# Performance work log

Hardware: AMD Instinct MI355X
Metric: run time of the kernel (lower is better)

Reference implementation:

```python
import jax, jax.numpy as jnp
import numpy as np

N = 100000          # nodes
E = 1600000         # edges (avg degree 16)
D_IN = 128          # in_features
D_OUT = 128         # out_features


def setup_inputs() -> dict:
    key = jax.random.key(0)
    k1, k2, k3, k4 = jax.random.split(key, 4)
    H = jax.random.normal(k1, (N, D_IN), dtype=jnp.float32)
    # COO indices of sparse adjacency A: row i aggregates features of col j
    src = jax.random.randint(k2, (E,), 0, N, dtype=jnp.int32)
    dst = jax.random.randint(k3, (E,), 0, N, dtype=jnp.int32)
    # nn.Linear(2*in_features, out_features): weight [out, 2*in], zero bias
    W = jax.random.normal(k4, (D_OUT, 2 * D_IN), dtype=jnp.float32) * 0.05
    b = jnp.zeros((D_OUT,), dtype=jnp.float32)
    return {"H": H, "src": src, "dst": dst, "W": W, "b": b}


def reference(H, src, dst, W, b):
    # max-aggregation: for each node i, max over features of its neighbors.
    # One fused gather + segment-max replaces the per-node Python loop.
    gathered = H[dst]  # [E, D_IN]
    agg = jax.ops.segment_max(gathered, src, num_segments=N)  # [N, D_IN]
    # nodes with no incoming edges stay zero (torch code leaves zeros)
    deg = jax.ops.segment_sum(jnp.ones((src.shape[0],), jnp.float32), src,
                              num_segments=N)  # [N]
    H_neigh = jnp.where(deg[:, None] > 0, agg, 0.0)
    H_concat = jnp.concatenate([H, H_neigh], axis=1)  # [N, 2*D_IN]
    return H_concat @ W.T + b
```

## Files before the change

kernel.cpp:

```cpp
#include <hip/hip_runtime.h>
#include <math.h>

#define NN 100000
#define NE 1600000
#define DD 128
#define NB 1563
#define CAP 1280
#define PB 196
#define CB 196

#define WS_HH  0
#define WS_CUR 6400000
#define WS_ENT (WS_CUR + NB)
#define WS_AH  (WS_ENT + NB * CAP)
#define WS_WH  (WS_AH + NN * (DD / 2))

typedef __attribute__((ext_vector_type(8))) _Float16 h8_t;
typedef __attribute__((ext_vector_type(4))) _Float16 h4_t;
typedef __attribute__((ext_vector_type(2))) _Float16 h2_t;
typedef __attribute__((ext_vector_type(4))) float f4_t;

__device__ __forceinline__ unsigned pk2h(float x, float y) {
    h2_t h;
    h.x = (_Float16)x;
    h.y = (_Float16)y;
    return *(unsigned*)&h;
}

__device__ __forceinline__ h4_t h4max(h4_t a, h4_t b) {
    return __builtin_elementwise_max(a, b);
}

__global__ __launch_bounds__(1024) void init_kernel(const float* __restrict__ W,
                                                    unsigned* __restrict__ Wh,
                                                    int* __restrict__ cursor) {
    int i = blockIdx.x * 1024 + threadIdx.x;
    if (i < 128 * 256 / 2) Wh[i] = pk2h(W[2 * i], W[2 * i + 1]);
    int j = i - 128 * 256 / 2;
    if (j >= 0 && j < NB) cursor[j] = 0;
}

__global__ __launch_bounds__(1024) void prep_kernel(const float* __restrict__ H,
                                                    const int* __restrict__ src,
                                                    const int* __restrict__ dst,
                                                    int* __restrict__ cursor,
                                                    unsigned* __restrict__ entries,
                                                    uint4* __restrict__ Hh4) {
    __shared__ int cnt[NB];
    __shared__ int gcur[NB];
    const int t = threadIdx.x;
    const int b = blockIdx.x;
    if (b < PB) {
        for (int i = t; i < NB; i += 1024) cnt[i] = 0;
        __syncthreads();
        const int base = b * 8192;
        int sv[8];
#pragma unroll
        for (int k = 0; k < 8; ++k) {
            int e = base + k * 1024 + t;
            sv[k] = (e < NE) ? src[e] : -1;
            if (sv[k] >= 0) atomicAdd(&cnt[sv[k] >> 6], 1);
        }
        __syncthreads();
        for (int i = t; i < NB; i += 1024) {
            int c = cnt[i];
            gcur[i] = c ? i * CAP + atomicAdd(&cursor[i], c) : 0;
        }
        __syncthreads();
#pragma unroll
        for (int k = 0; k < 8; ++k) {
            int e = base + k * 1024 + t;
            if (sv[k] >= 0) {
                int s = sv[k];
                int pos = atomicAdd(&gcur[s >> 6], 1);
                entries[pos] = ((unsigned)(s & 63) << 17) | (unsigned)dst[e];
            }
        }
    } else {
        const int nb = b - PB;
        const int n8 = NN * DD / 8;
        for (int i = nb * 1024 + t; i < n8; i += CB * 1024) {
            const float4* s = (const float4*)H + (size_t)i * 2;
            float4 a = s[0], c4 = s[1];
            uint4 o;
            o.x = pk2h(a.x, a.y);
            o.y = pk2h(a.z, a.w);
            o.z = pk2h(c4.x, c4.y);
            o.w = pk2h(c4.z, c4.w);
            Hh4[i] = o;
        }
    }
}

__global__ __launch_bounds__(256) void agg_kernel(const _Float16* __restrict__ Hh,
                                                  const int* __restrict__ cursor,
                                                  const unsigned* __restrict__ entries,
                                                  unsigned* __restrict__ Ah) {
    __shared__ unsigned raw[CAP];
    __shared__ unsigned sorted[CAP];
    __shared__ int cnt[64], base_s[64], cur[64];
    const int t = threadIdx.x;
    const int b = blockIdx.x;
    const int n = cursor[b];

    if (t < 64) cnt[t] = 0;
    __syncthreads();
    for (int i = t; i < n; i += 256) {
        unsigned e = entries[b * CAP + i];
        raw[i] = e;
        atomicAdd(&cnt[e >> 17], 1);
    }
    __syncthreads();
    if (t < 64) {
        int v = cnt[t];
        int incl = v;
#pragma unroll
        for (int o = 1; o < 64; o <<= 1) {
            int y = __shfl_up(incl, o, 64);
            if (t >= o) incl += y;
        }
        base_s[t] = incl - v;
        cur[t] = incl - v;
    }
    __syncthreads();
    for (int i = t; i < n; i += 256) {
        unsigned e = raw[i];
        int pos = atomicAdd(&cur[e >> 17], 1);
        sorted[pos] = e & 0x1FFFFu;
    }
    __syncthreads();

    const int lane = t & 63;
    const int w = t >> 6;
    const int half = lane >> 5;
    const int l32 = lane & 31;
    const _Float16* __restrict__ colbase = Hh + l32 * 4;
#pragma unroll
    for (int q = 0; q < 16; ++q) {
        int ln = w * 16 + q;
        int s0 = base_s[ln];
        int e0 = s0 + cnt[ln];
        unsigned long long mu = 0xFC00FC00FC00FC00ull;
        h4_t m = *(h4_t*)&mu;
        int j = s0 + half;
        for (; j + 6 < e0; j += 8) {
            int d0 = sorted[j], d1 = sorted[j + 2];
            int d2 = sorted[j + 4], d3 = sorted[j + 6];
            h4_t v0 = *(const h4_t*)(colbase + (size_t)d0 * DD);
            h4_t v1 = *(const h4_t*)(colbase + (size_t)d1 * DD);
            h4_t v2 = *(const h4_t*)(colbase + (size_t)d2 * DD);
            h4_t v3 = *(const h4_t*)(colbase + (size_t)d3 * DD);
            m = h4max(m, h4max(h4max(v0, v1), h4max(v2, v3)));
        }
        for (; j < e0; j += 2) {
            h4_t v0 = *(const h4_t*)(colbase + (size_t)sorted[j] * DD);
            m = h4max(m, v0);
        }
        uint2 mv = *(uint2*)&m;
        uint2 ov;
        ov.x = (unsigned)__shfl_xor((int)mv.x, 32, 64);
        ov.y = (unsigned)__shfl_xor((int)mv.y, 32, 64);
        h4_t om = *(h4_t*)&ov;
        m = h4max(m, om);
        int node = b * 64 + ln;
        if (half == 0 && node < NN) {
            uint2 outv = make_uint2(0u, 0u);
            if (s0 < e0) outv = *(uint2*)&m;
            *(uint2*)(Ah + (size_t)node * 64 + l32 * 2) = outv;
        }
    }
}

#define XP 72
__global__ __launch_bounds__(256) void mfma_matmul_kernel(
        const unsigned short* __restrict__ Hh,
        const unsigned short* __restrict__ Ah,
        const unsigned short* __restrict__ Wh,
        const float* __restrict__ bias,
        float* __restrict__ out) {
    __shared__ unsigned short Xs[128 * XP];
    __shared__ unsigned short Ws[128 * XP];
    const int t = threadIdx.x;
    const int lane = t & 63;
    const int w = t >> 6;
    const int quad = lane >> 4;
    const int l16 = lane & 15;
    const int blockrow = blockIdx.x * 128;

    f4_t acc[2][8] = {};

    for (int c = 0; c < 4; ++c) {
        const int k0 = c * 64;
        {
            const unsigned short* xb = (c < 2) ? Hh : Ah;
            const int koff = (c < 2) ? k0 : k0 - 128;
            const int seg = t & 7, r0 = t >> 3;
#pragma unroll
            for (int j = 0; j < 4; ++j) {
                int r = r0 + 32 * j;
                int row = blockrow + r;
                uint4 v = make_uint4(0, 0, 0, 0);
                if (row < NN)
                    v = *(const uint4*)(xb + (size_t)row * DD + koff + seg * 8);
                *(uint4*)&Xs[r * XP + seg * 8] = v;
            }
        }
        {
            const int seg = t & 7, o0 = t >> 3;
#pragma unroll
            for (int j = 0; j < 4; ++j) {
                int o = o0 + 32 * j;
                uint4 v = *(const uint4*)(Wh + (size_t)o * 256 + k0 + seg * 8);
                *(uint4*)&Ws[o * XP + seg * 8] = v;
            }
        }
        __syncthreads();
#pragma unroll
        for (int kk = 0; kk < 64; kk += 32) {
            h8_t a0 = *(const h8_t*)&Xs[(w * 32 + l16) * XP + kk + quad * 8];
            h8_t a1 = *(const h8_t*)&Xs[(w * 32 + 16 + l16) * XP + kk + quad * 8];
#pragma unroll
            for (int ot = 0; ot < 8; ++ot) {
                h8_t bf = *(const h8_t*)&Ws[(ot * 16 + l16) * XP + kk + quad * 8];
                acc[0][ot] = __builtin_amdgcn_mfma_f32_16x16x32_f16(a0, bf, acc[0][ot], 0, 0, 0);
                acc[1][ot] = __builtin_amdgcn_mfma_f32_16x16x32_f16(a1, bf, acc[1][ot], 0, 0, 0);
            }
        }
        __syncthreads();
    }

#pragma unroll
    for (int ot = 0; ot < 8; ++ot) {
        float bv = bias[ot * 16 + l16];
#pragma unroll
        for (int sub = 0; sub < 2; ++sub) {
#pragma unroll
            for (int reg = 0; reg < 4; ++reg) {
                int row = blockrow + w * 32 + sub * 16 + quad * 4 + reg;
                if (row < NN)
                    out[(size_t)row * DD + ot * 16 + l16] = acc[sub][ot][reg] + bv;
            }
        }
    }
}

extern "C" void kernel_launch(void* const* d_in, const int* in_sizes, int n_in,
                              void* d_out, int out_size, void* d_ws, size_t ws_size,
                              hipStream_t stream) {
    const float* H   = (const float*)d_in[0];
    const int*   src = (const int*)d_in[1];
    const int*   dst = (const int*)d_in[2];
    const float* W   = (const float*)d_in[3];
    const float* b   = (const float*)d_in[4];
    float* out = (float*)d_out;

    int* ws = (int*)d_ws;
    unsigned short* Hh      = (unsigned short*)(ws + WS_HH);
    int*            cursor  = ws + WS_CUR;
    unsigned*       entries = (unsigned*)(ws + WS_ENT);
    unsigned*       Ah      = (unsigned*)(ws + WS_AH);
    unsigned*       Wh      = (unsigned*)(ws + WS_WH);

    init_kernel<<<18, 1024, 0, stream>>>(W, Wh, cursor);
    prep_kernel<<<PB + CB, 1024, 0, stream>>>(H, src, dst, cursor, entries, (uint4*)Hh);
    agg_kernel<<<NB, 256, 0, stream>>>((const _Float16*)Hh, cursor, entries, Ah);
    mfma_matmul_kernel<<<(NN + 127) / 128, 256, 0, stream>>>(
        Hh, (const unsigned short*)Ah, (const unsigned short*)Wh, b, out);
}
```

Before: 238.3 us.

## Fuse neighbor max-aggregation with MFMA matmul and fold weight conversion into prep

Merges the aggregation kernel and the matmul kernel so each 64-node block keeps its aggregated half-precision features and its own H rows in shared memory, then runs the MFMA GEMM directly on them. This removes the global write and re-read of the aggregated buffer and one kernel launch. The weight-conversion init kernel is folded into an extra prep block and the cursor reset becomes a memset. The trade-off is a smaller 64-row matmul tile per block, so weights are reloaded once per 64 rows instead of per 128, and shared memory use rises, which may lower occupancy during the gather phase.

```diff
diff --git a/kernel.cpp b/kernel.cpp
--- a/kernel.cpp
+++ b/kernel.cpp
@@ -12,8 +12,7 @@
 #define WS_HH  0
 #define WS_CUR 6400000
 #define WS_ENT (WS_CUR + NB)
-#define WS_AH  (WS_ENT + NB * CAP)
-#define WS_WH  (WS_AH + NN * (DD / 2))
+#define WS_WH  (WS_ENT + NB * CAP)
 
 typedef __attribute__((ext_vector_type(8))) _Float16 h8_t;
 typedef __attribute__((ext_vector_type(4))) _Float16 h4_t;
@@ -31,21 +30,14 @@
     return __builtin_elementwise_max(a, b);
 }
 
-__global__ __launch_bounds__(1024) void init_kernel(const float* __restrict__ W,
-                                                    unsigned* __restrict__ Wh,
-                                                    int* __restrict__ cursor) {
-    int i = blockIdx.x * 1024 + threadIdx.x;
-    if (i < 128 * 256 / 2) Wh[i] = pk2h(W[2 * i], W[2 * i + 1]);
-    int j = i - 128 * 256 / 2;
-    if (j >= 0 && j < NB) cursor[j] = 0;
-}
-
 __global__ __launch_bounds__(1024) void prep_kernel(const float* __restrict__ H,
                                                     const int* __restrict__ src,
                                                     const int* __restrict__ dst,
                                                     int* __restrict__ cursor,
                                                     unsigned* __restrict__ entries,
-                                                    uint4* __restrict__ Hh4) {
+                                                    uint4* __restrict__ Hh4,
+                                                    const float* __restrict__ W,
+                                                    unsigned* __restrict__ Wh) {
     __shared__ int cnt[NB];
     __shared__ int gcur[NB];
     const int t = threadIdx.x;
@@ -76,7 +68,7 @@
                 entries[pos] = ((unsigned)(s & 63) << 17) | (unsigned)dst[e];
             }
         }
-    } else {
+    } else if (b < PB + CB) {
         const int nb = b - PB;
         const int n8 = NN * DD / 8;
         for (int i = nb * 1024 + t; i < n8; i += CB * 1024) {
@@ -89,15 +81,26 @@
             o.w = pk2h(c4.z, c4.w);
             Hh4[i] = o;
         }
-    }
-}
-
-__global__ __launch_bounds__(256) void agg_kernel(const _Float16* __restrict__ Hh,
-                                                  const int* __restrict__ cursor,
-                                                  const unsigned* __restrict__ entries,
-                                                  unsigned* __restrict__ Ah) {
-    __shared__ unsigned raw[CAP];
-    __shared__ unsigned sorted[CAP];
+    } else {
+        for (int i = t; i < 128 * 256 / 2; i += 1024)
+            Wh[i] = pk2h(W[2 * i], W[2 * i + 1]);
+    }
+}
+
+#define XP 72
+#define X64P 264
+__global__ __launch_bounds__(256) void aggmat_kernel(
+        const unsigned short* __restrict__ Hh,
+        const int* __restrict__ cursor,
+        const unsigned* __restrict__ entries,
+        const unsigned short* __restrict__ Wh,
+        const float* __restrict__ bias,
+        float* __restrict__ out) {
+    __shared__ __align__(16) unsigned short Xs[64 * X64P];
+    __shared__ __align__(16) union SU {
+        struct { unsigned raw[CAP]; unsigned sorted[CAP]; } s;
+        unsigned short Ws[128 * XP];
+    } u;
     __shared__ int cnt[64], base_s[64], cur[64];
     const int t = threadIdx.x;
     const int b = blockIdx.x;
@@ -107,7 +110,7 @@
     __syncthreads();
     for (int i = t; i < n; i += 256) {
         unsigned e = entries[b * CAP + i];
-        raw[i] = e;
+        u.s.raw[i] = e;
         atomicAdd(&cnt[e >> 17], 1);
     }
     __syncthreads();
@@ -124,17 +127,29 @@
     }
     __syncthreads();
     for (int i = t; i < n; i += 256) {
-        unsigned e = raw[i];
+        unsigned e = u.s.raw[i];
         int pos = atomicAdd(&cur[e >> 17], 1);
-        sorted[pos] = e & 0x1FFFFu;
-    }
-    __syncthreads();
+        u.s.sorted[pos] = e & 0x1FFFFu;
+    }
+    __syncthreads();
+
+    {
+        const int seg = t & 15, r0 = t >> 4;
+#pragma unroll
+        for (int j = 0; j < 4; ++j) {
+            int r = r0 + 16 * j;
+            int row = b * 64 + r;
+            uint4 v = make_uint4(0, 0, 0, 0);
+            if (row < NN) v = *(const uint4*)(Hh + (size_t)row * DD + seg * 8);
+            *(uint4*)&Xs[r * X64P + seg * 8] = v;
+        }
+    }
 
     const int lane = t & 63;
     const int w = t >> 6;
     const int half = lane >> 5;
     const int l32 = lane & 31;
-    const _Float16* __restrict__ colbase = Hh + l32 * 4;
+    const _Float16* __restrict__ colbase = (const _Float16*)Hh + l32 * 4;
 #pragma unroll
     for (int q = 0; q < 16; ++q) {
         int ln = w * 16 + q;
@@ -144,8 +159,8 @@
         h4_t m = *(h4_t*)&mu;
         int j = s0 + half;
         for (; j + 6 < e0; j += 8) {
-            int d0 = sorted[j], d1 = sorted[j + 2];
-            int d2 = sorted[j + 4], d3 = sorted[j + 6];
+            int d0 = u.s.sorted[j], d1 = u.s.sorted[j + 2];
+            int d2 = u.s.sorted[j + 4], d3 = u.s.sorted[j + 6];
             h4_t v0 = *(const h4_t*)(colbase + (size_t)d0 * DD);
             h4_t v1 = *(const h4_t*)(colbase + (size_t)d1 * DD);
             h4_t v2 = *(const h4_t*)(colbase + (size_t)d2 * DD);
@@ -153,7 +168,7 @@
             m = h4max(m, h4max(h4max(v0, v1), h4max(v2, v3)));
         }
         for (; j < e0; j += 2) {
-            h4_t v0 = *(const h4_t*)(colbase + (size_t)sorted[j] * DD);
+            h4_t v0 = *(const h4_t*)(colbase + (size_t)u.s.sorted[j] * DD);
             m = h4max(m, v0);
         }
         uint2 mv = *(uint2*)&m;
@@ -162,68 +177,35 @@
         ov.y = (unsigned)__shfl_xor((int)mv.y, 32, 64);
         h4_t om = *(h4_t*)&ov;
         m = h4max(m, om);
-        int node = b * 64 + ln;
-        if (half == 0 && node < NN) {
+        if (half == 0) {
             uint2 outv = make_uint2(0u, 0u);
             if (s0 < e0) outv = *(uint2*)&m;
-            *(uint2*)(Ah + (size_t)node * 64 + l32 * 2) = outv;
-        }
-    }
-}
-
-#define XP 72
-__global__ __launch_bounds__(256) void mfma_matmul_kernel(
-        const unsigned short* __restrict__ Hh,
-        const unsigned short* __restrict__ Ah,
-        const unsigned short* __restrict__ Wh,
-        const float* __restrict__ bias,
-        float* __restrict__ out) {
-    __shared__ unsigned short Xs[128 * XP];
-    __shared__ unsigned short Ws[128 * XP];
-    const int t = threadIdx.x;
-    const int lane = t & 63;
-    const int w = t >> 6;
+            *(uint2*)&Xs[ln * X64P + 128 + l32 * 4] = outv;
+        }
+    }
+    __syncthreads();
+
     const int quad = lane >> 4;
     const int l16 = lane & 15;
-    const int blockrow = blockIdx.x * 128;
-
-    f4_t acc[2][8] = {};
-
+    f4_t acc[8] = {};
     for (int c = 0; c < 4; ++c) {
-        const int k0 = c * 64;
-        {
-            const unsigned short* xb = (c < 2) ? Hh : Ah;
-            const int koff = (c < 2) ? k0 : k0 - 128;
-            const int seg = t & 7, r0 = t >> 3;
-#pragma unroll
-            for (int j = 0; j < 4; ++j) {
-                int r = r0 + 32 * j;
-                int row = blockrow + r;
-                uint4 v = make_uint4(0, 0, 0, 0);
-                if (row < NN)
-                    v = *(const uint4*)(xb + (size_t)row * DD + koff + seg * 8);
-                *(uint4*)&Xs[r * XP + seg * 8] = v;
-            }
-        }
         {
             const int seg = t & 7, o0 = t >> 3;
 #pragma unroll
             for (int j = 0; j < 4; ++j) {
                 int o = o0 + 32 * j;
-                uint4 v = *(const uint4*)(Wh + (size_t)o * 256 + k0 + seg * 8);
-                *(uint4*)&Ws[o * XP + seg * 8] = v;
+                uint4 v = *(const uint4*)(Wh + (size_t)o * 256 + c * 64 + seg * 8);
+                *(uint4*)&u.Ws[o * XP + seg * 8] = v;
             }
         }
         __syncthreads();
 #pragma unroll
         for (int kk = 0; kk < 64; kk += 32) {
-            h8_t a0 = *(const h8_t*)&Xs[(w * 32 + l16) * XP + kk + quad * 8];
-            h8_t a1 = *(const h8_t*)&Xs[(w * 32 + 16 + l16) * XP + kk + quad * 8];
+            h8_t a = *(const h8_t*)&Xs[(w * 16 + l16) * X64P + c * 64 + kk + quad * 8];
 #pragma unroll
             for (int ot = 0; ot < 8; ++ot) {
-                h8_t bf = *(const h8_t*)&Ws[(ot * 16 + l16) * XP + kk + quad * 8];
-                acc[0][ot] = __builtin_amdgcn_mfma_f32_16x16x32_f16(a0, bf, acc[0][ot], 0, 0, 0);
-                acc[1][ot] = __builtin_amdgcn_mfma_f32_16x16x32_f16(a1, bf, acc[1][ot], 0, 0, 0);
+                h8_t bf = *(const h8_t*)&u.Ws[(ot * 16 + l16) * XP + kk + quad * 8];
+                acc[ot] = __builtin_amdgcn_mfma_f32_16x16x32_f16(a, bf, acc[ot], 0, 0, 0);
             }
         }
         __syncthreads();
@@ -233,13 +215,10 @@
     for (int ot = 0; ot < 8; ++ot) {
         float bv = bias[ot * 16 + l16];
 #pragma unroll
-        for (int sub = 0; sub < 2; ++sub) {
-#pragma unroll
-            for (int reg = 0; reg < 4; ++reg) {
-                int row = blockrow + w * 32 + sub * 16 + quad * 4 + reg;
-                if (row < NN)
-                    out[(size_t)row * DD + ot * 16 + l16] = acc[sub][ot][reg] + bv;
-            }
+        for (int reg = 0; reg < 4; ++reg) {
+            int row = b * 64 + w * 16 + quad * 4 + reg;
+            if (row < NN)
+                out[(size_t)row * DD + ot * 16 + l16] = acc[ot][reg] + bv;
         }
     }
 }
@@ -258,12 +237,12 @@
     unsigned short* Hh      = (unsigned short*)(ws + WS_HH);
     int*            cursor  = ws + WS_CUR;
     unsigned*       entries = (unsigned*)(ws + WS_ENT);
-    unsigned*       Ah      = (unsigned*)(ws + WS_AH);
     unsigned*       Wh      = (unsigned*)(ws + WS_WH);
 
-    init_kernel<<<18, 1024, 0, stream>>>(W, Wh, cursor);
-    prep_kernel<<<PB + CB, 1024, 0, stream>>>(H, src, dst, cursor, entries, (uint4*)Hh);
-    agg_kernel<<<NB, 256, 0, stream>>>((const _Float16*)Hh, cursor, entries, Ah);
-    mfma_matmul_kernel<<<(NN + 127) / 128, 256, 0, stream>>>(
-        Hh, (const unsigned short*)Ah, (const unsigned short*)Wh, b, out);
-}
+    hipMemsetAsync(cursor, 0, NB * sizeof(int), stream);
+    prep_kernel<<<PB + CB + 1, 1024, 0, stream>>>(H, src, dst, cursor, entries,
+                                                  (uint4*)Hh, W, Wh);
+    aggmat_kernel<<<NB, 256, 0, stream>>>(
+        (const unsigned short*)Hh, cursor, entries,
+        (const unsigned short*)Wh, b, out);
+}
```

New measurement: 253.0 us. +6.2%, slower.

## Halve aggregation bin size, fold weight conversion into prep, drop LDS in matmul

Applied to the files above, without the earlier changes.

Edges are now bucketed into 32-node bins instead of 64-node bins, which doubles the number of aggregation blocks and halves per-block work and shared-memory capacity. This is meant to improve load balance and occupancy. The separate init kernel is replaced by a memset plus an extra prep block that converts W to fp16, saving a launch. The matmul drops its LDS staging and syncs: each wave reads A rows and W fragments straight from global memory into MFMA operands over 64-row tiles. This relies on cache hits for W reuse, and the smaller CAP raises the risk of bin overflow.

```diff
diff --git a/kernel.cpp b/kernel.cpp
--- a/kernel.cpp
+++ b/kernel.cpp
@@ -4,15 +4,15 @@
 #define NN 100000
 #define NE 1600000
 #define DD 128
-#define NB 1563
-#define CAP 1280
+#define NBINS 3125
+#define CAP 640
 #define PB 196
 #define CB 196
 
 #define WS_HH  0
 #define WS_CUR 6400000
-#define WS_ENT (WS_CUR + NB)
-#define WS_AH  (WS_ENT + NB * CAP)
+#define WS_ENT (WS_CUR + NBINS)
+#define WS_AH  (WS_ENT + NBINS * CAP)
 #define WS_WH  (WS_AH + NN * (DD / 2))
 
 typedef __attribute__((ext_vector_type(8))) _Float16 h8_t;
@@ -31,27 +31,20 @@
     return __builtin_elementwise_max(a, b);
 }
 
-__global__ __launch_bounds__(1024) void init_kernel(const float* __restrict__ W,
-                                                    unsigned* __restrict__ Wh,
-                                                    int* __restrict__ cursor) {
-    int i = blockIdx.x * 1024 + threadIdx.x;
-    if (i < 128 * 256 / 2) Wh[i] = pk2h(W[2 * i], W[2 * i + 1]);
-    int j = i - 128 * 256 / 2;
-    if (j >= 0 && j < NB) cursor[j] = 0;
-}
-
 __global__ __launch_bounds__(1024) void prep_kernel(const float* __restrict__ H,
                                                     const int* __restrict__ src,
                                                     const int* __restrict__ dst,
                                                     int* __restrict__ cursor,
                                                     unsigned* __restrict__ entries,
-                                                    uint4* __restrict__ Hh4) {
-    __shared__ int cnt[NB];
-    __shared__ int gcur[NB];
+                                                    uint4* __restrict__ Hh4,
+                                                    const float* __restrict__ W,
+                                                    unsigned* __restrict__ Wh) {
+    __shared__ int cnt[NBINS];
+    __shared__ int gcur[NBINS];
     const int t = threadIdx.x;
     const int b = blockIdx.x;
     if (b < PB) {
-        for (int i = t; i < NB; i += 1024) cnt[i] = 0;
+        for (int i = t; i < NBINS; i += 1024) cnt[i] = 0;
         __syncthreads();
         const int base = b * 8192;
         int sv[8];
@@ -59,10 +52,10 @@
         for (int k = 0; k < 8; ++k) {
             int e = base + k * 1024 + t;
             sv[k] = (e < NE) ? src[e] : -1;
-            if (sv[k] >= 0) atomicAdd(&cnt[sv[k] >> 6], 1);
+            if (sv[k] >= 0) atomicAdd(&cnt[sv[k] >> 5], 1);
         }
         __syncthreads();
-        for (int i = t; i < NB; i += 1024) {
+        for (int i = t; i < NBINS; i += 1024) {
             int c = cnt[i];
             gcur[i] = c ? i * CAP + atomicAdd(&cursor[i], c) : 0;
         }
@@ -72,11 +65,11 @@
             int e = base + k * 1024 + t;
             if (sv[k] >= 0) {
                 int s = sv[k];
-                int pos = atomicAdd(&gcur[s >> 6], 1);
-                entries[pos] = ((unsigned)(s & 63) << 17) | (unsigned)dst[e];
+                int pos = atomicAdd(&gcur[s >> 5], 1);
+                entries[pos] = ((unsigned)(s & 31) << 17) | (unsigned)dst[e];
             }
         }
-    } else {
+    } else if (b < PB + CB) {
         const int nb = b - PB;
         const int n8 = NN * DD / 8;
         for (int i = nb * 1024 + t; i < n8; i += CB * 1024) {
@@ -89,6 +82,9 @@
             o.w = pk2h(c4.z, c4.w);
             Hh4[i] = o;
         }
+    } else {
+        for (int i = t; i < 128 * 256 / 2; i += 1024)
+            Wh[i] = pk2h(W[2 * i], W[2 * i + 1]);
     }
 }
 
@@ -98,12 +94,12 @@
                                                   unsigned* __restrict__ Ah) {
     __shared__ unsigned raw[CAP];
     __shared__ unsigned sorted[CAP];
-    __shared__ int cnt[64], base_s[64], cur[64];
+    __shared__ int cnt[32], base_s[32], cur[32];
     const int t = threadIdx.x;
     const int b = blockIdx.x;
     const int n = cursor[b];
 
-    if (t < 64) cnt[t] = 0;
+    if (t < 32) cnt[t] = 0;
     __syncthreads();
     for (int i = t; i < n; i += 256) {
         unsigned e = entries[b * CAP + i];
@@ -111,12 +107,12 @@
         atomicAdd(&cnt[e >> 17], 1);
     }
     __syncthreads();
-    if (t < 64) {
+    if (t < 32) {
         int v = cnt[t];
         int incl = v;
 #pragma unroll
-        for (int o = 1; o < 64; o <<= 1) {
-            int y = __shfl_up(incl, o, 64);
+        for (int o = 1; o < 32; o <<= 1) {
+            int y = __shfl_up(incl, o, 32);
             if (t >= o) incl += y;
         }
         base_s[t] = incl - v;
@@ -136,8 +132,8 @@
     const int l32 = lane & 31;
     const _Float16* __restrict__ colbase = Hh + l32 * 4;
 #pragma unroll
-    for (int q = 0; q < 16; ++q) {
-        int ln = w * 16 + q;
+    for (int q = 0; q < 8; ++q) {
+        int ln = w * 8 + q;
         int s0 = base_s[ln];
         int e0 = s0 + cnt[ln];
         unsigned long long mu = 0xFC00FC00FC00FC00ull;
@@ -162,7 +158,7 @@
         ov.y = (unsigned)__shfl_xor((int)mv.y, 32, 64);
         h4_t om = *(h4_t*)&ov;
         m = h4max(m, om);
-        int node = b * 64 + ln;
+        int node = b * 32 + ln;
         if (half == 0 && node < NN) {
             uint2 outv = make_uint2(0u, 0u);
             if (s0 < e0) outv = *(uint2*)&m;
@@ -171,75 +167,48 @@
     }
 }
 
-#define XP 72
 __global__ __launch_bounds__(256) void mfma_matmul_kernel(
         const unsigned short* __restrict__ Hh,
         const unsigned short* __restrict__ Ah,
         const unsigned short* __restrict__ Wh,
         const float* __restrict__ bias,
         float* __restrict__ out) {
-    __shared__ unsigned short Xs[128 * XP];
-    __shared__ unsigned short Ws[128 * XP];
     const int t = threadIdx.x;
     const int lane = t & 63;
     const int w = t >> 6;
     const int quad = lane >> 4;
     const int l16 = lane & 15;
-    const int blockrow = blockIdx.x * 128;
-
-    f4_t acc[2][8] = {};
-
+    const int arow = blockIdx.x * 64 + w * 16 + l16;
+    const bool aok = arow < NN;
+
+    f4_t acc[8] = {};
+#pragma unroll
     for (int c = 0; c < 4; ++c) {
-        const int k0 = c * 64;
-        {
-            const unsigned short* xb = (c < 2) ? Hh : Ah;
-            const int koff = (c < 2) ? k0 : k0 - 128;
-            const int seg = t & 7, r0 = t >> 3;
-#pragma unroll
-            for (int j = 0; j < 4; ++j) {
-                int r = r0 + 32 * j;
-                int row = blockrow + r;
-                uint4 v = make_uint4(0, 0, 0, 0);
-                if (row < NN)
-                    v = *(const uint4*)(xb + (size_t)row * DD + koff + seg * 8);
-                *(uint4*)&Xs[r * XP + seg * 8] = v;
+        const unsigned short* xb = (c < 2) ? Hh : Ah;
+        const int koff = (c & 1) * 64;
+#pragma unroll
+        for (int kk = 0; kk < 64; kk += 32) {
+            uint4 av = make_uint4(0, 0, 0, 0);
+            if (aok)
+                av = *(const uint4*)(xb + (size_t)arow * DD + koff + kk + quad * 8);
+            h8_t a = *(h8_t*)&av;
+#pragma unroll
+            for (int ot = 0; ot < 8; ++ot) {
+                h8_t bf = *(const h8_t*)(Wh + (size_t)(ot * 16 + l16) * 256
+                                         + c * 64 + kk + quad * 8);
+                acc[ot] = __builtin_amdgcn_mfma_f32_16x16x32_f16(a, bf, acc[ot], 0, 0, 0);
             }
         }
-        {
-            const int seg = t & 7, o0 = t >> 3;
-#pragma unroll
-            for (int j = 0; j < 4; ++j) {
-                int o = o0 + 32 * j;
-                uint4 v = *(const uint4*)(Wh + (size_t)o * 256 + k0 + seg * 8);
-                *(uint4*)&Ws[o * XP + seg * 8] = v;
-            }
-        }
-        __syncthreads();
-#pragma unroll
-        for (int kk = 0; kk < 64; kk += 32) {
-            h8_t a0 = *(const h8_t*)&Xs[(w * 32 + l16) * XP + kk + quad * 8];
-            h8_t a1 = *(const h8_t*)&Xs[(w * 32 + 16 + l16) * XP + kk + quad * 8];
-#pragma unroll
-            for (int ot = 0; ot < 8; ++ot) {
-                h8_t bf = *(const h8_t*)&Ws[(ot * 16 + l16) * XP + kk + quad * 8];
-                acc[0][ot] = __builtin_amdgcn_mfma_f32_16x16x32_f16(a0, bf, acc[0][ot], 0, 0, 0);
-                acc[1][ot] = __builtin_amdgcn_mfma_f32_16x16x32_f16(a1, bf, acc[1][ot], 0, 0, 0);
-            }
-        }
-        __syncthreads();
     }
 
 #pragma unroll
     for (int ot = 0; ot < 8; ++ot) {
         float bv = bias[ot * 16 + l16];
 #pragma unroll
-        for (int sub = 0; sub < 2; ++sub) {
-#pragma unroll
-            for (int reg = 0; reg < 4; ++reg) {
-                int row = blockrow + w * 32 + sub * 16 + quad * 4 + reg;
-                if (row < NN)
-                    out[(size_t)row * DD + ot * 16 + l16] = acc[sub][ot][reg] + bv;
-            }
+        for (int reg = 0; reg < 4; ++reg) {
+            int row = blockIdx.x * 64 + w * 16 + quad * 4 + reg;
+            if (row < NN)
+                out[(size_t)row * DD + ot * 16 + l16] = acc[ot][reg] + bv;
         }
     }
 }
@@ -261,9 +230,10 @@
     unsigned*       Ah      = (unsigned*)(ws + WS_AH);
     unsigned*       Wh      = (unsigned*)(ws + WS_WH);
 
-    init_kernel<<<18, 1024, 0, stream>>>(W, Wh, cursor);
-    prep_kernel<<<PB + CB, 1024, 0, stream>>>(H, src, dst, cursor, entries, (uint4*)Hh);
-    agg_kernel<<<NB, 256, 0, stream>>>((const _Float16*)Hh, cursor, entries, Ah);
-    mfma_matmul_kernel<<<(NN + 127) / 128, 256, 0, stream>>>(
+    hipMemsetAsync(cursor, 0, NBINS * sizeof(int), stream);
+    prep_kernel<<<PB + CB + 1, 1024, 0, stream>>>(H, src, dst, cursor, entries,
+                                                  (uint4*)Hh, W, Wh);
+    agg_kernel<<<NBINS, 256, 0, stream>>>((const _Float16*)Hh, cursor, entries, Ah);
+    mfma_matmul_kernel<<<(NN + 63) / 64, 256, 0, stream>>>(
         Hh, (const unsigned short*)Ah, (const unsigned short*)Wh, b, out);
 }
```

Result: slower. 264.0 us (+10.8%).

## Fuse all stages into one cooperative persistent kernel with grid syncs

Applied to the files above, without the earlier changes.

Replaces the four separate launches (init, prep, agg, matmul) with a single cooperative mega-kernel of 768 blocks that uses grid.sync between phases. It loops persistently over bins and 64-row matmul tiles, and overlays the shared memory of all phases in one union. The aim is to remove launch gaps and the tail idle time between kernels. In exchange it adds three grid-wide barriers and cuts per-block parallelism (256 threads, a smaller matmul tile that reloads W per tile). If the cooperative launch fails, it falls back to the old multi-kernel path.

```diff
diff --git a/kernel.cpp b/kernel.cpp
--- a/kernel.cpp
+++ b/kernel.cpp
@@ -1,13 +1,19 @@
 #include <hip/hip_runtime.h>
+#include <hip/hip_cooperative_groups.h>
 #include <math.h>
+
+namespace cg = cooperative_groups;
 
 #define NN 100000
 #define NE 1600000
 #define DD 128
 #define NB 1563
 #define CAP 1280
+#define NBLK 768
+#define PVB 392
 #define PB 196
-#define CB 196
+#define CB 392
+#define XP 72
 
 #define WS_HH  0
 #define WS_CUR 6400000
@@ -31,13 +37,204 @@
     return __builtin_elementwise_max(a, b);
 }
 
-__global__ __launch_bounds__(1024) void init_kernel(const float* __restrict__ W,
-                                                    unsigned* __restrict__ Wh,
-                                                    int* __restrict__ cursor) {
-    int i = blockIdx.x * 1024 + threadIdx.x;
-    if (i < 128 * 256 / 2) Wh[i] = pk2h(W[2 * i], W[2 * i + 1]);
-    int j = i - 128 * 256 / 2;
-    if (j >= 0 && j < NB) cursor[j] = 0;
+__global__ __launch_bounds__(256, 4) void mega_kernel(
+        const float* __restrict__ H,
+        const int* __restrict__ src,
+        const int* __restrict__ dst,
+        const float* __restrict__ W,
+        const float* __restrict__ bias,
+        int* __restrict__ cursor,
+        unsigned* __restrict__ entries,
+        unsigned short* __restrict__ Hh,
+        unsigned* __restrict__ Ah,
+        unsigned short* __restrict__ Wh,
+        float* __restrict__ out) {
+    cg::grid_group grid = cg::this_grid();
+    __shared__ __align__(16) union LU {
+        struct { int cnt[NB]; int gcur[NB]; } p;
+        struct { unsigned raw[CAP]; unsigned sorted[CAP];
+                 int cnt[64], base[64], cur[64]; } a;
+        unsigned short Ws[128 * XP];
+    } L;
+    const int t = threadIdx.x;
+    const int b = blockIdx.x;
+    const int G = gridDim.x;
+
+    {
+        int i = b * 256 + t;
+        if (i < NB) cursor[i] = 0;
+    }
+    __threadfence();
+    grid.sync();
+
+    if (b < PVB) {
+        for (int i = t; i < NB; i += 256) L.p.cnt[i] = 0;
+        __syncthreads();
+        const int base = b * 4096;
+        int sv[16];
+#pragma unroll
+        for (int k = 0; k < 16; ++k) {
+            int e = base + k * 256 + t;
+            sv[k] = (e < NE) ? src[e] : -1;
+            if (sv[k] >= 0) atomicAdd(&L.p.cnt[sv[k] >> 6], 1);
+        }
+        __syncthreads();
+        for (int i = t; i < NB; i += 256) {
+            int c = L.p.cnt[i];
+            L.p.gcur[i] = c ? i * CAP + atomicAdd(&cursor[i], c) : 0;
+        }
+        __syncthreads();
+#pragma unroll
+        for (int k = 0; k < 16; ++k) {
+            if (sv[k] >= 0) {
+                int e = base + k * 256 + t;
+                int s = sv[k];
+                int pos = atomicAdd(&L.p.gcur[s >> 6], 1);
+                entries[pos] = ((unsigned)(s & 63) << 17) | (unsigned)dst[e];
+            }
+        }
+    } else if (b < G - 1) {
+        const int nconv = G - 1 - PVB;
+        const int nb = b - PVB;
+        const int n8 = NN * DD / 8;
+        const float4* Hf = (const float4*)H;
+        uint4* Hh4 = (uint4*)Hh;
+        for (int i = nb * 256 + t; i < n8; i += nconv * 256) {
+            float4 x = Hf[2 * i], y = Hf[2 * i + 1];
+            uint4 o;
+            o.x = pk2h(x.x, x.y);
+            o.y = pk2h(x.z, x.w);
+            o.z = pk2h(y.x, y.y);
+            o.w = pk2h(y.z, y.w);
+            Hh4[i] = o;
+        }
+    } else {
+        unsigned* Wh32 = (unsigned*)Wh;
+        for (int i = t; i < 128 * 256 / 2; i += 256)
+            Wh32[i] = pk2h(W[2 * i], W[2 * i + 1]);
+    }
+    __threadfence();
+    grid.sync();
+
+    for (int bin = b; bin < NB; bin += G) {
+        __syncthreads();
+        const int n = cursor[bin];
+        if (t < 64) L.a.cnt[t] = 0;
+        __syncthreads();
+        for (int i = t; i < n; i += 256) {
+            unsigned e = entries[bin * CAP + i];
+            L.a.raw[i] = e;
+            atomicAdd(&L.a.cnt[e >> 17], 1);
+        }
+        __syncthreads();
+        if (t < 64) {
+            int v = L.a.cnt[t];
+            int incl = v;
+#pragma unroll
+            for (int o = 1; o < 64; o <<= 1) {
+                int y = __shfl_up(incl, o, 64);
+                if (t >= o) incl += y;
+            }
+            L.a.base[t] = incl - v;
+            L.a.cur[t] = incl - v;
+        }
+        __syncthreads();
+        for (int i = t; i < n; i += 256) {
+            unsigned e = L.a.raw[i];
+            int pos = atomicAdd(&L.a.cur[e >> 17], 1);
+            L.a.sorted[pos] = e & 0x1FFFFu;
+        }
+        __syncthreads();
+
+        const int lane = t & 63;
+        const int w = t >> 6;
+        const int half = lane >> 5;
+        const int l32 = lane & 31;
+        const _Float16* __restrict__ colbase = (const _Float16*)Hh + l32 * 4;
+#pragma unroll
+        for (int q = 0; q < 16; ++q) {
+            int ln = w * 16 + q;
+            int s0 = L.a.base[ln];
+            int e0 = s0 + L.a.cnt[ln];
+            unsigned long long mu = 0xFC00FC00FC00FC00ull;
+            h4_t m = *(h4_t*)&mu;
+            int j = s0 + half;
+            for (; j + 6 < e0; j += 8) {
+                int d0 = L.a.sorted[j], d1 = L.a.sorted[j + 2];
+                int d2 = L.a.sorted[j + 4], d3 = L.a.sorted[j + 6];
+                h4_t v0 = *(const h4_t*)(colbase + (size_t)d0 * DD);
+                h4_t v1 = *(const h4_t*)(colbase + (size_t)d1 * DD);
+                h4_t v2 = *(const h4_t*)(colbase + (size_t)d2 * DD);
+                h4_t v3 = *(const h4_t*)(colbase + (size_t)d3 * DD);
+                m = h4max(m, h4max(h4max(v0, v1), h4max(v2, v3)));
+            }
+            for (; j < e0; j += 2) {
+                h4_t v0 = *(const h4_t*)(colbase + (size_t)L.a.sorted[j] * DD);
+                m = h4max(m, v0);
+            }
+            uint2 mv = *(uint2*)&m;
+            uint2 ov;
+            ov.x = (unsigned)__shfl_xor((int)mv.x, 32, 64);
+            ov.y = (unsigned)__shfl_xor((int)mv.y, 32, 64);
+            h4_t om = *(h4_t*)&ov;
+            m = h4max(m, om);
+            int node = bin * 64 + ln;
+            if (half == 0 && node < NN) {
+                uint2 outv = make_uint2(0u, 0u);
+                if (s0 < e0) outv = *(uint2*)&m;
+                *(uint2*)(Ah + (size_t)node * 64 + l32 * 2) = outv;
+            }
+        }
+    }
+    __threadfence();
+    grid.sync();
+
+    for (int tile = b; tile < (NN + 63) / 64; tile += G) {
+        const int lane = t & 63;
+        const int w = t >> 6;
+        const int quad = lane >> 4;
+        const int l16 = lane & 15;
+        const int arow = tile * 64 + w * 16 + l16;
+        f4_t acc[8] = {};
+#pragma unroll
+        for (int c = 0; c < 4; ++c) {
+            __syncthreads();
+            {
+                const int seg = t & 7, o0 = t >> 3;
+#pragma unroll
+                for (int j = 0; j < 4; ++j) {
+                    int o = o0 + 32 * j;
+                    *(uint4*)&L.Ws[o * XP + seg * 8] =
+                        *(const uint4*)(Wh + (size_t)o * 256 + c * 64 + seg * 8);
+                }
+            }
+            __syncthreads();
+            const unsigned short* xb = (c < 2) ? Hh : (const unsigned short*)Ah;
+            const int koff = (c & 1) * 64;
+#pragma unroll
+            for (int kk = 0; kk < 64; kk += 32) {
+                uint4 av = make_uint4(0, 0, 0, 0);
+                if (arow < NN)
+                    av = *(const uint4*)(xb + (size_t)arow * DD + koff + kk + quad * 8);
+                h8_t a = *(h8_t*)&av;
+#pragma unroll
+                for (int ot = 0; ot < 8; ++ot) {
+                    h8_t bf = *(const h8_t*)&L.Ws[(ot * 16 + l16) * XP + kk + quad * 8];
+                    acc[ot] = __builtin_amdgcn_mfma_f32_16x16x32_f16(a, bf, acc[ot], 0, 0, 0);
+                }
+            }
+        }
+#pragma unroll
+        for (int ot = 0; ot < 8; ++ot) {
+            float bv = bias[ot * 16 + l16];
+#pragma unroll
+            for (int reg = 0; reg < 4; ++reg) {
+                int row = tile * 64 + w * 16 + quad * 4 + reg;
+                if (row < NN)
+                    out[(size_t)row * DD + ot * 16 + l16] = acc[ot][reg] + bv;
+            }
+        }
+    }
 }
 
 __global__ __launch_bounds__(1024) void prep_kernel(const float* __restrict__ H,
@@ -45,7 +242,9 @@
                                                     const int* __restrict__ dst,
                                                     int* __restrict__ cursor,
                                                     unsigned* __restrict__ entries,
-                                                    uint4* __restrict__ Hh4) {
+                                                    uint4* __restrict__ Hh4,
+                                                    const float* __restrict__ W,
+                                                    unsigned* __restrict__ Wh) {
     __shared__ int cnt[NB];
     __shared__ int gcur[NB];
     const int t = threadIdx.x;
@@ -76,7 +275,7 @@
                 entries[pos] = ((unsigned)(s & 63) << 17) | (unsigned)dst[e];
             }
         }
-    } else {
+    } else if (b < PB + CB) {
         const int nb = b - PB;
         const int n8 = NN * DD / 8;
         for (int i = nb * 1024 + t; i < n8; i += CB * 1024) {
@@ -89,6 +288,9 @@
             o.w = pk2h(c4.z, c4.w);
             Hh4[i] = o;
         }
+    } else {
+        for (int i = t; i < 128 * 256 / 2; i += 1024)
+            Wh[i] = pk2h(W[2 * i], W[2 * i + 1]);
     }
 }
 
@@ -171,7 +373,6 @@
     }
 }
 
-#define XP 72
 __global__ __launch_bounds__(256) void mfma_matmul_kernel(
         const unsigned short* __restrict__ Hh,
         const unsigned short* __restrict__ Ah,
@@ -247,11 +448,11 @@
 extern "C" void kernel_launch(void* const* d_in, const int* in_sizes, int n_in,
                               void* d_out, int out_size, void* d_ws, size_t ws_size,
                               hipStream_t stream) {
-    const float* H   = (const float*)d_in[0];
-    const int*   src = (const int*)d_in[1];
-    const int*   dst = (const int*)d_in[2];
-    const float* W   = (const float*)d_in[3];
-    const float* b   = (const float*)d_in[4];
+    const float* H    = (const float*)d_in[0];
+    const int*   src  = (const int*)d_in[1];
+    const int*   dst  = (const int*)d_in[2];
+    const float* W    = (const float*)d_in[3];
+    const float* bias = (const float*)d_in[4];
     float* out = (float*)d_out;
 
     int* ws = (int*)d_ws;
@@ -259,11 +460,22 @@
     int*            cursor  = ws + WS_CUR;
     unsigned*       entries = (unsigned*)(ws + WS_ENT);
     unsigned*       Ah      = (unsigned*)(ws + WS_AH);
-    unsigned*       Wh      = (unsigned*)(ws + WS_WH);
-
-    init_kernel<<<18, 1024, 0, stream>>>(W, Wh, cursor);
-    prep_kernel<<<PB + CB, 1024, 0, stream>>>(H, src, dst, cursor, entries, (uint4*)Hh);
-    agg_kernel<<<NB, 256, 0, stream>>>((const _Float16*)Hh, cursor, entries, Ah);
-    mfma_matmul_kernel<<<(NN + 127) / 128, 256, 0, stream>>>(
-        Hh, (const unsigned short*)Ah, (const unsigned short*)Wh, b, out);
-}
+    unsigned short* Wh      = (unsigned short*)(ws + WS_WH);
+
+    void* args[] = {(void*)&H, (void*)&src, (void*)&dst, (void*)&W, (void*)&bias,
+                    (void*)&cursor, (void*)&entries, (void*)&Hh, (void*)&Ah,
+                    (void*)&Wh, (void*)&out};
+    hipError_t err = hipLaunchCooperativeKernel((const void*)mega_kernel,
+                                                dim3(NBLK), dim3(256),
+                                                args, 0, stream);
+    if (err != hipSuccess) {
+        (void)hipGetLastError();
+        hipMemsetAsync(cursor, 0, NB * sizeof(int), stream);
+        prep_kernel<<<PB + CB + 1, 1024, 0, stream>>>(H, src, dst, cursor,
+                                                      entries, (uint4*)Hh, W,
+                                                      (unsigned*)Wh);
+        agg_kernel<<<NB, 256, 0, stream>>>((const _Float16*)Hh, cursor, entries, Ah);
+        mfma_matmul_kernel<<<(NN + 127) / 128, 256, 0, stream>>>(
+            Hh, (const unsigned short*)Ah, Wh, bias, out);
+    }
+}
```

Result: slower. 700.2 us (+193.8%).
